# Optimization experiments

Hardware: AMD Instinct MI355X
Metric: run time of the kernel (lower is better)

Reference implementation:

```python
import jax, jax.numpy as jnp
import numpy as np

N = 4096          # num_tracks
NTOP = 4          # n neighbours
OUT_DIM = 32
EMB = OUT_DIM // NTOP  # 8, Linear(4 -> 8)


def setup_inputs() -> dict:
    key = jax.random.key(0)
    k1, k2, k3, k4 = jax.random.split(key, 4)
    obs1 = jax.random.normal(k1, (N, 2), dtype=jnp.float32)
    obs2 = jax.random.normal(k2, (N, 2), dtype=jnp.float32)
    # Linear weight stored as [in, out] = [4, 8] (torch uses [out, in]; math is x @ W + b)
    W = jax.random.normal(k3, (4, EMB), dtype=jnp.float32) * 0.5
    b = jax.random.normal(k4, (EMB,), dtype=jnp.float32) * 0.1
    return {"obs1": obs1, "obs2": obs2, "W": W, "b": b}


def _offdiag_index(n):
    # idx[i, j] = column index of the j-th off-diagonal element in row i
    cols = jnp.arange(n - 1)
    rows = jnp.arange(n)[:, None]
    return cols[None, :] + (cols[None, :] >= rows).astype(jnp.int32)  # [n, n-1]


def reference(obs1, obs2, W, b):
    n = obs2.shape[0]
    # pairwise relative position / velocity: rel[i, j] = other_j - self_i
    rel_pos_full = obs2[None, :, :] - obs2[:, None, :]        # [N, N, 2]
    vel = obs2 - obs1
    rel_vel_full = vel[None, :, :] - vel[:, None, :]          # [N, N, 2]

    idx = _offdiag_index(n)                                   # [N, N-1]
    rel_pos = jnp.take_along_axis(rel_pos_full, idx[:, :, None], axis=1)  # [N, N-1, 2]
    rel_vel = jnp.take_along_axis(rel_vel_full, idx[:, :, None], axis=1)  # [N, N-1, 2]
    grid = jnp.concatenate([rel_pos, rel_vel], axis=2)        # [N, N-1, 4]

    dist = jnp.linalg.norm(rel_pos, axis=2)                   # [N, N-1]
    _, di = jax.lax.top_k(-dist, NTOP)                        # [N, NTOP] nearest
    nearest = jnp.take_along_axis(grid, di[:, :, None], axis=1)  # [N, NTOP, 4]

    h = jax.nn.relu(nearest @ W + b)                          # [N, NTOP, EMB]
    return h.reshape(n, NTOP * EMB)                           # [N, 32]
```

## Files before the change

### kernel.cpp

```cpp
#include <hip/hip_runtime.h>
#include <float.h>

#define NT 4096
#define NTOP 4
#define EMB 8

#define LEXLT(da, ja, db, jb) (((da) < (db)) || (((da) == (db)) && ((ja) < (jb))))

__global__ __launch_bounds__(256) void nn_pool_kernel(
    const float* __restrict__ obs1,
    const float* __restrict__ obs2,
    const float* __restrict__ W,
    const float* __restrict__ bias,
    float* __restrict__ out)
{
    __shared__ float2 s_pos[NT];

    const int tid = threadIdx.x;
    const float2* g_pos = reinterpret_cast<const float2*>(obs2);
    #pragma unroll
    for (int k = 0; k < NT / 256; ++k)
        s_pos[tid + k * 256] = g_pos[tid + k * 256];
    __syncthreads();

    const int wave = tid >> 6;
    const int lane = tid & 63;
    const int row  = (blockIdx.x << 2) + wave;

    const float2 pi = s_pos[row];

    float bd0 = FLT_MAX, bd1 = FLT_MAX, bd2 = FLT_MAX, bd3 = FLT_MAX;
    int   bj0 = 0x7fffffff, bj1 = 0x7fffffff, bj2 = 0x7fffffff, bj3 = 0x7fffffff;

    #pragma unroll 4
    for (int k = 0; k < NT / 64; ++k) {
        const int j = lane + (k << 6);
        const float2 pj = s_pos[j];
        const float dx = __fsub_rn(pj.x, pi.x);
        const float dy = __fsub_rn(pj.y, pi.y);
        const float d2 = __fadd_rn(__fmul_rn(dx, dx), __fmul_rn(dy, dy));
        float d = __fsqrt_rn(d2);
        if (j == row) d = FLT_MAX;

        const bool c3 = d < bd3;
        const bool c2 = d < bd2;
        const bool c1 = d < bd1;
        const bool c0 = d < bd0;
        bd3 = c3 ? (c2 ? bd2 : d) : bd3;   bj3 = c3 ? (c2 ? bj2 : j) : bj3;
        bd2 = c2 ? (c1 ? bd1 : d) : bd2;   bj2 = c2 ? (c1 ? bj1 : j) : bj2;
        bd1 = c1 ? (c0 ? bd0 : d) : bd1;   bj1 = c1 ? (c0 ? bj0 : j) : bj1;
        bd0 = c0 ? d : bd0;                bj0 = c0 ? j : bj0;
    }

    #pragma unroll
    for (int off = 1; off < 64; off <<= 1) {
        const float od0 = __shfl_xor(bd0, off, 64);
        const float od1 = __shfl_xor(bd1, off, 64);
        const float od2 = __shfl_xor(bd2, off, 64);
        const float od3 = __shfl_xor(bd3, off, 64);
        const int   oj0 = __shfl_xor(bj0, off, 64);
        const int   oj1 = __shfl_xor(bj1, off, 64);
        const int   oj2 = __shfl_xor(bj2, off, 64);
        const int   oj3 = __shfl_xor(bj3, off, 64);

        float l0, l1, l2, l3; int m0, m1, m2, m3;
        { const bool t = LEXLT(od3, oj3, bd0, bj0); l0 = t ? od3 : bd0; m0 = t ? oj3 : bj0; }
        { const bool t = LEXLT(od2, oj2, bd1, bj1); l1 = t ? od2 : bd1; m1 = t ? oj2 : bj1; }
        { const bool t = LEXLT(od1, oj1, bd2, bj2); l2 = t ? od1 : bd2; m2 = t ? oj1 : bj2; }
        { const bool t = LEXLT(od0, oj0, bd3, bj3); l3 = t ? od0 : bd3; m3 = t ? oj0 : bj3; }

        { const bool t = LEXLT(l2, m2, l0, m0); float td=l0; int tj=m0;
          if (t) { l0=l2; m0=m2; l2=td; m2=tj; } }
        { const bool t = LEXLT(l3, m3, l1, m1); float td=l1; int tj=m1;
          if (t) { l1=l3; m1=m3; l3=td; m3=tj; } }
        { const bool t = LEXLT(l1, m1, l0, m0); float td=l0; int tj=m0;
          if (t) { l0=l1; m0=m1; l1=td; m1=tj; } }
        { const bool t = LEXLT(l3, m3, l2, m2); float td=l2; int tj=m2;
          if (t) { l2=l3; m2=m3; l3=td; m3=tj; } }

        bd0 = l0; bd1 = l1; bd2 = l2; bd3 = l3;
        bj0 = m0; bj1 = m1; bj2 = m2; bj3 = m3;
    }

    if (lane < 32) {
        const int t = lane >> 3;
        const int e = lane & 7;
        int j = (t == 0) ? bj0 : (t == 1) ? bj1 : (t == 2) ? bj2 : bj3;
        j &= (NT - 1);

        const float2 pj = s_pos[j];
        const float2* g_o1 = reinterpret_cast<const float2*>(obs1);
        const float2 o1j = g_o1[j];
        const float2 o1i = g_o1[row];

        const float dx  = pj.x - pi.x;
        const float dy  = pj.y - pi.y;
        const float vjx = pj.x - o1j.x;
        const float vjy = pj.y - o1j.y;
        const float vix = pi.x - o1i.x;
        const float viy = pi.y - o1i.y;
        const float dvx = vjx - vix;
        const float dvy = vjy - viy;

        float acc = bias[e]
                  + dx  * W[0 * EMB + e]
                  + dy  * W[1 * EMB + e]
                  + dvx * W[2 * EMB + e]
                  + dvy * W[3 * EMB + e];
        out[row * 32 + lane] = fmaxf(acc, 0.0f);
    }
}

extern "C" void kernel_launch(void* const* d_in, const int* in_sizes, int n_in,
                              void* d_out, int out_size, void* d_ws, size_t ws_size,
                              hipStream_t stream) {
    const float* obs1 = nullptr;
    const float* obs2 = nullptr;
    const float* W    = nullptr;
    const float* bias = nullptr;
    int big_seen = 0;
    for (int i = 0; i < n_in; ++i) {
        if (in_sizes[i] == 2 * NT) {
            if (big_seen++ == 0) obs1 = (const float*)d_in[i];
            else                 obs2 = (const float*)d_in[i];
        } else if (in_sizes[i] == 4 * EMB) {
            W = (const float*)d_in[i];
        } else if (in_sizes[i] == EMB) {
            bias = (const float*)d_in[i];
        }
    }
    if (!obs1 || !obs2 || !W || !bias) {
        obs1 = (const float*)d_in[0];
        obs2 = (const float*)d_in[1];
        W    = (const float*)d_in[2];
        bias = (const float*)d_in[3];
    }
    float* out = (float*)d_out;

    nn_pool_kernel<<<NT / 4, 256, 0, stream>>>(obs1, obs2, W, bias, out);
}
```

Baseline: 77.45 us.

## Split each row across two waves, read positions directly, pack keys for shuffles

Each row's neighbour scan is now split across two waves that each cover half of the tracks, and the two partial top-4 lists are merged through a small shared array. The full LDS staging of all positions is removed. Each lane instead reads float4 pairs of positions straight from global memory and keeps two independent top-4 lists to add instruction-level parallelism. Distance and index are packed into a 64-bit key so the shuffle merge uses unsigned compares instead of lexicographic float/int logic. The grid doubles, so twice as many waves run with less serial work each, at the cost of an extra block sync and merge and reliance on cache hits for the global reads.

```diff
diff --git a/kernel.cpp b/kernel.cpp
--- a/kernel.cpp
+++ b/kernel.cpp
@@ -2,10 +2,25 @@
 #include <float.h>
 
 #define NT 4096
-#define NTOP 4
 #define EMB 8
 
+typedef unsigned long long u64;
+typedef unsigned int u32;
+
 #define LEXLT(da, ja, db, jb) (((da) < (db)) || (((da) == (db)) && ((ja) < (jb))))
+
+#define CESWAP(dx, jx, dy, jy) do {                                   \
+    const bool t_ = LEXLT(dy, jy, dx, jx);                            \
+    const float td_ = t_ ? dy : dx;  const int tj_ = t_ ? jy : jx;    \
+    dy = t_ ? dx : dy;  jy = t_ ? jx : jy;                            \
+    dx = td_;           jx = tj_;                                     \
+} while (0)
+
+__device__ __forceinline__ u64 shfl_xor_u64(u64 v, int off) {
+    const int lo = __shfl_xor((int)(v & 0xFFFFFFFFull), off, 64);
+    const int hi = __shfl_xor((int)(v >> 32), off, 64);
+    return ((u64)(u32)hi << 32) | (u32)lo;
+}
 
 __global__ __launch_bounds__(256) void nn_pool_kernel(
     const float* __restrict__ obs1,
@@ -14,93 +29,113 @@
     const float* __restrict__ bias,
     float* __restrict__ out)
 {
-    __shared__ float2 s_pos[NT];
+    __shared__ u64 s_top[4][4];
 
-    const int tid = threadIdx.x;
-    const float2* g_pos = reinterpret_cast<const float2*>(obs2);
-    #pragma unroll
-    for (int k = 0; k < NT / 256; ++k)
-        s_pos[tid + k * 256] = g_pos[tid + k * 256];
-    __syncthreads();
+    const int tid  = threadIdx.x;
+    const int w    = tid >> 6;
+    const int lane = tid & 63;
+    const int row  = (blockIdx.x << 1) + (w >> 1);
+    const int h    = w & 1;
 
-    const int wave = tid >> 6;
-    const int lane = tid & 63;
-    const int row  = (blockIdx.x << 2) + wave;
+    const float2 pi = reinterpret_cast<const float2*>(obs2)[row];
 
-    const float2 pi = s_pos[row];
+    float dA0=FLT_MAX,dA1=FLT_MAX,dA2=FLT_MAX,dA3=FLT_MAX;
+    float dB0=FLT_MAX,dB1=FLT_MAX,dB2=FLT_MAX,dB3=FLT_MAX;
+    int   jA0=0x7fffffff,jA1=0x7fffffff,jA2=0x7fffffff,jA3=0x7fffffff;
+    int   jB0=0x7fffffff,jB1=0x7fffffff,jB2=0x7fffffff,jB3=0x7fffffff;
 
-    float bd0 = FLT_MAX, bd1 = FLT_MAX, bd2 = FLT_MAX, bd3 = FLT_MAX;
-    int   bj0 = 0x7fffffff, bj1 = 0x7fffffff, bj2 = 0x7fffffff, bj3 = 0x7fffffff;
+    const float4* pos4 = reinterpret_cast<const float4*>(obs2);
+    const int fbase = (h << 10) + lane;
 
     #pragma unroll 4
-    for (int k = 0; k < NT / 64; ++k) {
-        const int j = lane + (k << 6);
-        const float2 pj = s_pos[j];
-        const float dx = __fsub_rn(pj.x, pi.x);
-        const float dy = __fsub_rn(pj.y, pi.y);
-        const float d2 = __fadd_rn(__fmul_rn(dx, dx), __fmul_rn(dy, dy));
-        float d = __fsqrt_rn(d2);
-        if (j == row) d = FLT_MAX;
+    for (int k = 0; k < 16; ++k) {
+        const float4 v = pos4[fbase + (k << 6)];
+        const int j0 = (h << 11) + (k << 7) + (lane << 1);
+        const int j1 = j0 + 1;
+        {
+            const float dx = __fsub_rn(v.x, pi.x);
+            const float dy = __fsub_rn(v.y, pi.y);
+            float d = __fsqrt_rn(__fadd_rn(__fmul_rn(dx,dx), __fmul_rn(dy,dy)));
+            if (j0 == row) d = FLT_MAX;
+            const bool c3 = d < dA3, c2 = d < dA2, c1 = d < dA1, c0 = d < dA0;
+            dA3 = c3 ? (c2 ? dA2 : d) : dA3;   jA3 = c3 ? (c2 ? jA2 : j0) : jA3;
+            dA2 = c2 ? (c1 ? dA1 : d) : dA2;   jA2 = c2 ? (c1 ? jA1 : j0) : jA2;
+            dA1 = c1 ? (c0 ? dA0 : d) : dA1;   jA1 = c1 ? (c0 ? jA0 : j0) : jA1;
+            dA0 = c0 ? d : dA0;                jA0 = c0 ? j0 : jA0;
+        }
+        {
+            const float dx = __fsub_rn(v.z, pi.x);
+            const float dy = __fsub_rn(v.w, pi.y);
+            float d = __fsqrt_rn(__fadd_rn(__fmul_rn(dx,dx), __fmul_rn(dy,dy)));
+            if (j1 == row) d = FLT_MAX;
+            const bool c3 = d < dB3, c2 = d < dB2, c1 = d < dB1, c0 = d < dB0;
+            dB3 = c3 ? (c2 ? dB2 : d) : dB3;   jB3 = c3 ? (c2 ? jB2 : j1) : jB3;
+            dB2 = c2 ? (c1 ? dB1 : d) : dB2;   jB2 = c2 ? (c1 ? jB1 : j1) : jB2;
+            dB1 = c1 ? (c0 ? dB0 : d) : dB1;   jB1 = c1 ? (c0 ? jB0 : j1) : jB1;
+            dB0 = c0 ? d : dB0;                jB0 = c0 ? j1 : jB0;
+        }
+    }
 
-        const bool c3 = d < bd3;
-        const bool c2 = d < bd2;
-        const bool c1 = d < bd1;
-        const bool c0 = d < bd0;
-        bd3 = c3 ? (c2 ? bd2 : d) : bd3;   bj3 = c3 ? (c2 ? bj2 : j) : bj3;
-        bd2 = c2 ? (c1 ? bd1 : d) : bd2;   bj2 = c2 ? (c1 ? bj1 : j) : bj2;
-        bd1 = c1 ? (c0 ? bd0 : d) : bd1;   bj1 = c1 ? (c0 ? bj0 : j) : bj1;
-        bd0 = c0 ? d : bd0;                bj0 = c0 ? j : bj0;
-    }
+    float l0, l1, l2, l3; int m0, m1, m2, m3;
+    { const bool t = LEXLT(dB3,jB3,dA0,jA0); l0 = t?dB3:dA0; m0 = t?jB3:jA0; }
+    { const bool t = LEXLT(dB2,jB2,dA1,jA1); l1 = t?dB2:dA1; m1 = t?jB2:jA1; }
+    { const bool t = LEXLT(dB1,jB1,dA2,jA2); l2 = t?dB1:dA2; m2 = t?jB1:jA2; }
+    { const bool t = LEXLT(dB0,jB0,dA3,jA3); l3 = t?dB0:dA3; m3 = t?jB0:jA3; }
+    CESWAP(l0,m0,l2,m2); CESWAP(l1,m1,l3,m3); CESWAP(l0,m0,l1,m1); CESWAP(l2,m2,l3,m3);
+
+    u64 k0 = ((u64)__float_as_uint(l0) << 32) | (u32)m0;
+    u64 k1 = ((u64)__float_as_uint(l1) << 32) | (u32)m1;
+    u64 k2 = ((u64)__float_as_uint(l2) << 32) | (u32)m2;
+    u64 k3 = ((u64)__float_as_uint(l3) << 32) | (u32)m3;
 
     #pragma unroll
     for (int off = 1; off < 64; off <<= 1) {
-        const float od0 = __shfl_xor(bd0, off, 64);
-        const float od1 = __shfl_xor(bd1, off, 64);
-        const float od2 = __shfl_xor(bd2, off, 64);
-        const float od3 = __shfl_xor(bd3, off, 64);
-        const int   oj0 = __shfl_xor(bj0, off, 64);
-        const int   oj1 = __shfl_xor(bj1, off, 64);
-        const int   oj2 = __shfl_xor(bj2, off, 64);
-        const int   oj3 = __shfl_xor(bj3, off, 64);
-
-        float l0, l1, l2, l3; int m0, m1, m2, m3;
-        { const bool t = LEXLT(od3, oj3, bd0, bj0); l0 = t ? od3 : bd0; m0 = t ? oj3 : bj0; }
-        { const bool t = LEXLT(od2, oj2, bd1, bj1); l1 = t ? od2 : bd1; m1 = t ? oj2 : bj1; }
-        { const bool t = LEXLT(od1, oj1, bd2, bj2); l2 = t ? od1 : bd2; m2 = t ? oj1 : bj2; }
-        { const bool t = LEXLT(od0, oj0, bd3, bj3); l3 = t ? od0 : bd3; m3 = t ? oj0 : bj3; }
-
-        { const bool t = LEXLT(l2, m2, l0, m0); float td=l0; int tj=m0;
-          if (t) { l0=l2; m0=m2; l2=td; m2=tj; } }
-        { const bool t = LEXLT(l3, m3, l1, m1); float td=l1; int tj=m1;
-          if (t) { l1=l3; m1=m3; l3=td; m3=tj; } }
-        { const bool t = LEXLT(l1, m1, l0, m0); float td=l0; int tj=m0;
-          if (t) { l0=l1; m0=m1; l1=td; m1=tj; } }
-        { const bool t = LEXLT(l3, m3, l2, m2); float td=l2; int tj=m2;
-          if (t) { l2=l3; m2=m3; l3=td; m3=tj; } }
-
-        bd0 = l0; bd1 = l1; bd2 = l2; bd3 = l3;
-        bj0 = m0; bj1 = m1; bj2 = m2; bj3 = m3;
+        const u64 p0 = shfl_xor_u64(k0, off);
+        const u64 p1 = shfl_xor_u64(k1, off);
+        const u64 p2 = shfl_xor_u64(k2, off);
+        const u64 p3 = shfl_xor_u64(k3, off);
+        u64 a0 = k0 < p3 ? k0 : p3;
+        u64 a1 = k1 < p2 ? k1 : p2;
+        u64 a2 = k2 < p1 ? k2 : p1;
+        u64 a3 = k3 < p0 ? k3 : p0;
+        { const u64 t = a0 < a2 ? a0 : a2; a2 = a0 < a2 ? a2 : a0; a0 = t; }
+        { const u64 t = a1 < a3 ? a1 : a3; a3 = a1 < a3 ? a3 : a1; a1 = t; }
+        { const u64 t = a0 < a1 ? a0 : a1; a1 = a0 < a1 ? a1 : a0; a0 = t; }
+        { const u64 t = a2 < a3 ? a2 : a3; a3 = a2 < a3 ? a3 : a2; a2 = t; }
+        k0 = a0; k1 = a1; k2 = a2; k3 = a3;
     }
 
-    if (lane < 32) {
+    if (lane < 4)
+        s_top[w][lane] = (lane == 0) ? k0 : (lane == 1) ? k1 : (lane == 2) ? k2 : k3;
+    __syncthreads();
+
+    const int pw = w ^ 1;
+    const u64 q0 = s_top[pw][0], q1 = s_top[pw][1], q2 = s_top[pw][2], q3 = s_top[pw][3];
+    u64 a0 = k0 < q3 ? k0 : q3;
+    u64 a1 = k1 < q2 ? k1 : q2;
+    u64 a2 = k2 < q1 ? k2 : q1;
+    u64 a3 = k3 < q0 ? k3 : q0;
+    { const u64 t = a0 < a2 ? a0 : a2; a2 = a0 < a2 ? a2 : a0; a0 = t; }
+    { const u64 t = a1 < a3 ? a1 : a3; a3 = a1 < a3 ? a3 : a1; a1 = t; }
+    { const u64 t = a0 < a1 ? a0 : a1; a1 = a0 < a1 ? a1 : a0; a0 = t; }
+    { const u64 t = a2 < a3 ? a2 : a3; a3 = a2 < a3 ? a3 : a2; a2 = t; }
+
+    if (h == 0 && lane < 32) {
         const int t = lane >> 3;
         const int e = lane & 7;
-        int j = (t == 0) ? bj0 : (t == 1) ? bj1 : (t == 2) ? bj2 : bj3;
-        j &= (NT - 1);
+        const u64 key = (t == 0) ? a0 : (t == 1) ? a1 : (t == 2) ? a2 : a3;
+        const int j = (int)((u32)key) & (NT - 1);
 
-        const float2 pj = s_pos[j];
-        const float2* g_o1 = reinterpret_cast<const float2*>(obs1);
+        const float2* g_pos = reinterpret_cast<const float2*>(obs2);
+        const float2* g_o1  = reinterpret_cast<const float2*>(obs1);
+        const float2 pj  = g_pos[j];
         const float2 o1j = g_o1[j];
         const float2 o1i = g_o1[row];
 
         const float dx  = pj.x - pi.x;
         const float dy  = pj.y - pi.y;
-        const float vjx = pj.x - o1j.x;
-        const float vjy = pj.y - o1j.y;
-        const float vix = pi.x - o1i.x;
-        const float viy = pi.y - o1i.y;
-        const float dvx = vjx - vix;
-        const float dvy = vjy - viy;
+        const float dvx = (pj.x - o1j.x) - (pi.x - o1i.x);
+        const float dvy = (pj.y - o1j.y) - (pi.y - o1i.y);
 
         float acc = bias[e]
                   + dx  * W[0 * EMB + e]
@@ -137,5 +172,5 @@
     }
     float* out = (float*)d_out;
 
-    nn_pool_kernel<<<NT / 4, 256, 0, stream>>>(obs1, obs2, W, bias, out);
+    nn_pool_kernel<<<NT / 2, 256, 0, stream>>>(obs1, obs2, W, bias, out);
 }
```

After: 79.00 us. +2.0%, slower.
